# Kernel optimization log

Measured on AMD Instinct MI355X. Metric: run time of the kernel, lower is better.

## Reference

```python
import jax, jax.numpy as jnp
import numpy as np


def setup_inputs() -> dict:
    key = jax.random.key(0)
    k_adj, k_ann, k_b = jax.random.split(key, 3)
    B, N, F = 8, 4096, 64
    # Adjacency: sparse-ish nonnegative matrix (TF version stores it as tf.sparse;
    raw = jax.random.uniform(k_adj, (B, N, N), dtype=jnp.float32)
    adjacent = jnp.where(raw > 0.95, raw, 0.0)
    annotations = jax.random.normal(k_ann, (B, N, F), dtype=jnp.float32)
    bias = jax.random.normal(k_b, (1, 1, F), dtype=jnp.float32)
    return {"adjacent": adjacent, "annotations": annotations, "bias": bias}


def reference(adjacent, annotations, bias):
    # Per-batch sparse @ dense matmul in TF == batched matmul here.
    # adjacent: [B,N,N], annotations: [B,N,F] -> [B,N,F]
    out = jnp.einsum('bnm,bmf->bnf', adjacent, annotations)
    return out + bias
```

## Files before the change

kernel.cpp:

```cpp
#include <hip/hip_runtime.h>
#include <stdint.h>

typedef __bf16 bf16x8 __attribute__((ext_vector_type(8)));
typedef float f32x16 __attribute__((ext_vector_type(16)));

#define NN 4096
#define FF 64
#define BM 64
#define BK 128
#define NSTEP (NN / BK)

__device__ __forceinline__ unsigned short f2bf(float x) {
    unsigned int u = __builtin_bit_cast(unsigned int, x);
    unsigned int r = u + 0x7fffu + ((u >> 16) & 1u);
    return (unsigned short)(r >> 16);
}

__global__ __launch_bounds__(256) void annT_kernel(const float* __restrict__ ann,
                                                   unsigned short* __restrict__ annT) {
    __shared__ unsigned short tile[FF * 66];
    int b = blockIdx.x >> 6;
    int m0 = (blockIdx.x & 63) << 6;
    int t = threadIdx.x;
    int f = t & 63;
    int ml = t >> 6;
    const float* src = ann + ((size_t)(b * NN + m0)) * FF;
#pragma unroll
    for (int it = 0; it < 16; ++it) {
        int m = it * 4 + ml;
        tile[f * 66 + m] = f2bf(src[(size_t)m * FF + f]);
    }
    __syncthreads();
    int m2 = (t & 31) * 2;
    int fr = t >> 5;
    unsigned short* dst = annT + (size_t)b * FF * NN + m0;
#pragma unroll
    for (int it = 0; it < 8; ++it) {
        int fo = it * 8 + fr;
        unsigned int lo = tile[fo * 66 + m2];
        unsigned int hi = tile[fo * 66 + m2 + 1];
        *(unsigned int*)(dst + (size_t)fo * NN + m2) = lo | (hi << 16);
    }
}

__global__ __launch_bounds__(256, 2) void gconv_kernel(const float* __restrict__ A,
                                                       const unsigned short* __restrict__ annT,
                                                       const float* __restrict__ bias,
                                                       float* __restrict__ out) {
    __shared__ unsigned short sA[2][BM * BK];
    __shared__ unsigned short sB[2][FF * BK];

    int bi = blockIdx.x;
    int lw = (bi & 7) * 64 + (bi >> 3);
    int b = lw >> 6;
    int n0 = (lw & 63) << 6;

    int t = threadIdx.x;
    int lane = t & 63;
    int wid = t >> 6;
    int wm = wid >> 1;
    int wf = wid & 1;

    const float* Ab = A + (size_t)b * NN * NN + (size_t)n0 * NN;
    const unsigned short* Tb = annT + (size_t)b * FF * NN;

    float4 ra[8];
    uint4 rb[4];

    auto loadTiles = [&](int s) {
        int k0 = s * BK;
#pragma unroll
        for (int i = 0; i < 8; ++i) {
            int idx = i * 256 + t;
            int row = idx >> 5, c4 = idx & 31;
            ra[i] = *(const float4*)(Ab + (size_t)row * NN + k0 + c4 * 4);
        }
#pragma unroll
        for (int i = 0; i < 4; ++i) {
            int idx = i * 256 + t;
            int fr = idx >> 4, c8 = idx & 15;
            rb[i] = *(const uint4*)(Tb + (size_t)fr * NN + k0 + c8 * 8);
        }
    };

    auto writeLDS = [&](int bufi) {
        unsigned short* pA = sA[bufi];
        unsigned short* pB = sB[bufi];
#pragma unroll
        for (int i = 0; i < 8; ++i) {
            int idx = i * 256 + t;
            int row = idx >> 5, c4 = idx & 31;
            unsigned int byte = (unsigned)(row * 256 + c4 * 8);
            byte ^= (unsigned)((row & 15) << 4);
            ushort4 w;
            w.x = f2bf(ra[i].x);
            w.y = f2bf(ra[i].y);
            w.z = f2bf(ra[i].z);
            w.w = f2bf(ra[i].w);
            *(ushort4*)((char*)pA + byte) = w;
        }
#pragma unroll
        for (int i = 0; i < 4; ++i) {
            int idx = i * 256 + t;
            int fr = idx >> 4, c8 = idx & 15;
            unsigned int byte = (unsigned)(fr * 256 + c8 * 16);
            byte ^= (unsigned)((fr & 15) << 4);
            *(uint4*)((char*)pB + byte) = rb[i];
        }
    };

    int arow = wm * 32 + (lane & 31);
    unsigned aBase = (unsigned)(arow * 256);
    unsigned aswz = (unsigned)((arow & 15) << 4);
    int frow = wf * 32 + (lane & 31);
    unsigned bBase = (unsigned)(frow * 256);
    unsigned bswz = (unsigned)((frow & 15) << 4);
    unsigned kh = (unsigned)((lane >> 5) * 16);

    f32x16 acc = {};

    loadTiles(0);
    writeLDS(0);
    __syncthreads();

    for (int s = 0; s < NSTEP; ++s) {
        int cur = s & 1;
        if (s + 1 < NSTEP) loadTiles(s + 1);
        const char* pA = (const char*)sA[cur];
        const char* pB = (const char*)sB[cur];
#pragma unroll
        for (int ks = 0; ks < 8; ++ks) {
            unsigned ab = (aBase + (unsigned)(ks * 32) + kh) ^ aswz;
            unsigned bb = (bBase + (unsigned)(ks * 32) + kh) ^ bswz;
            bf16x8 af = *(const bf16x8*)(pA + ab);
            bf16x8 bfr = *(const bf16x8*)(pB + bb);
            acc = __builtin_amdgcn_mfma_f32_32x32x16_bf16(af, bfr, acc, 0, 0, 0);
        }
        if (s + 1 < NSTEP) writeLDS((s + 1) & 1);
        __syncthreads();
    }

    float bv = bias[wf * 32 + (lane & 31)];
    float* ob = out + ((size_t)(b * NN + n0 + wm * 32)) * FF + wf * 32 + (lane & 31);
    int rbase = (lane >> 5) * 4;
#pragma unroll
    for (int r = 0; r < 16; ++r) {
        int rowl = (r & 3) + 8 * (r >> 2) + rbase;
        ob[(size_t)rowl * FF] = acc[r] + bv;
    }
}

extern "C" void kernel_launch(void* const* d_in, const int* in_sizes, int n_in,
                              void* d_out, int out_size, void* d_ws, size_t ws_size,
                              hipStream_t stream) {
    const float* adj = (const float*)d_in[0];
    const float* ann = (const float*)d_in[1];
    const float* bias = (const float*)d_in[2];
    float* out = (float*)d_out;
    unsigned short* annT = (unsigned short*)d_ws;

    annT_kernel<<<dim3(8 * (NN / 64)), dim3(256), 0, stream>>>(ann, annT);
    gconv_kernel<<<dim3(8 * (NN / BM)), dim3(256), 0, stream>>>(adj, annT, bias, out);
}
```

Baseline: 686.1 us.

## Replace LDS-tiled GEMM with single-wave register-direct MFMA loads and double buffering

```diff
diff --git a/kernel.cpp b/kernel.cpp
--- a/kernel.cpp
+++ b/kernel.cpp
@@ -6,14 +6,15 @@
 
 #define NN 4096
 #define FF 64
-#define BM 64
-#define BK 128
-#define NSTEP (NN / BK)
 
 __device__ __forceinline__ unsigned short f2bf(float x) {
     unsigned int u = __builtin_bit_cast(unsigned int, x);
     unsigned int r = u + 0x7fffu + ((u >> 16) & 1u);
     return (unsigned short)(r >> 16);
+}
+
+__device__ __forceinline__ unsigned int pk2(float lo, float hi) {
+    return (unsigned int)f2bf(lo) | ((unsigned int)f2bf(hi) << 16);
 }
 
 __global__ __launch_bounds__(256) void annT_kernel(const float* __restrict__ ann,
@@ -43,110 +44,68 @@
     }
 }
 
-__global__ __launch_bounds__(256, 2) void gconv_kernel(const float* __restrict__ A,
-                                                       const unsigned short* __restrict__ annT,
-                                                       const float* __restrict__ bias,
-                                                       float* __restrict__ out) {
-    __shared__ unsigned short sA[2][BM * BK];
-    __shared__ unsigned short sB[2][FF * BK];
+__global__ __launch_bounds__(64) void gconv_kernel(const float* __restrict__ A,
+                                                   const unsigned short* __restrict__ annT,
+                                                   const float* __restrict__ bias,
+                                                   float* __restrict__ out) {
+    int bi = blockIdx.x;
+    int b = bi & 7;
+    int n0 = (bi >> 3) << 5;
+    int lane = threadIdx.x;
+    int r = lane & 31;
+    int h = lane >> 5;
 
-    int bi = blockIdx.x;
-    int lw = (bi & 7) * 64 + (bi >> 3);
-    int b = lw >> 6;
-    int n0 = (lw & 63) << 6;
+    const float* Ap = A + (size_t)b * NN * NN + (size_t)(n0 + r) * NN + h * 8;
+    const unsigned short* B0p = annT + (size_t)b * FF * NN + (size_t)r * NN + h * 8;
+    const unsigned short* B1p = B0p + (size_t)32 * NN;
 
-    int t = threadIdx.x;
-    int lane = t & 63;
-    int wid = t >> 6;
-    int wm = wid >> 1;
-    int wf = wid & 1;
+    f32x16 acc0 = {}, acc1 = {};
 
-    const float* Ab = A + (size_t)b * NN * NN + (size_t)n0 * NN;
-    const unsigned short* Tb = annT + (size_t)b * FF * NN;
+    float4 aA[4][2]; uint4 bA0[4], bA1[4];
+    float4 aB[4][2]; uint4 bB0[4], bB1[4];
 
-    float4 ra[8];
-    uint4 rb[4];
-
-    auto loadTiles = [&](int s) {
-        int k0 = s * BK;
+    auto loadSet = [&](float4 (&a)[4][2], uint4 (&b0)[4], uint4 (&b1)[4], int k0) {
 #pragma unroll
-        for (int i = 0; i < 8; ++i) {
-            int idx = i * 256 + t;
-            int row = idx >> 5, c4 = idx & 31;
-            ra[i] = *(const float4*)(Ab + (size_t)row * NN + k0 + c4 * 4);
+        for (int j = 0; j < 4; ++j) {
+            int k = k0 + j * 16;
+            a[j][0] = *(const float4*)(Ap + k);
+            a[j][1] = *(const float4*)(Ap + k + 4);
+            b0[j] = *(const uint4*)(B0p + k);
+            b1[j] = *(const uint4*)(B1p + k);
         }
+    };
+    auto compSet = [&](float4 (&a)[4][2], uint4 (&b0)[4], uint4 (&b1)[4]) {
 #pragma unroll
-        for (int i = 0; i < 4; ++i) {
-            int idx = i * 256 + t;
-            int fr = idx >> 4, c8 = idx & 15;
-            rb[i] = *(const uint4*)(Tb + (size_t)fr * NN + k0 + c8 * 8);
+        for (int j = 0; j < 4; ++j) {
+            uint4 ap;
+            ap.x = pk2(a[j][0].x, a[j][0].y);
+            ap.y = pk2(a[j][0].z, a[j][0].w);
+            ap.z = pk2(a[j][1].x, a[j][1].y);
+            ap.w = pk2(a[j][1].z, a[j][1].w);
+            bf16x8 af = __builtin_bit_cast(bf16x8, ap);
+            acc0 = __builtin_amdgcn_mfma_f32_32x32x16_bf16(
+                af, __builtin_bit_cast(bf16x8, b0[j]), acc0, 0, 0, 0);
+            acc1 = __builtin_amdgcn_mfma_f32_32x32x16_bf16(
+                af, __builtin_bit_cast(bf16x8, b1[j]), acc1, 0, 0, 0);
         }
     };
 
-    auto writeLDS = [&](int bufi) {
-        unsigned short* pA = sA[bufi];
-        unsigned short* pB = sB[bufi];
-#pragma unroll
-        for (int i = 0; i < 8; ++i) {
-            int idx = i * 256 + t;
-            int row = idx >> 5, c4 = idx & 31;
-            unsigned int byte = (unsigned)(row * 256 + c4 * 8);
-            byte ^= (unsigned)((row & 15) << 4);
-            ushort4 w;
-            w.x = f2bf(ra[i].x);
-            w.y = f2bf(ra[i].y);
-            w.z = f2bf(ra[i].z);
-            w.w = f2bf(ra[i].w);
-            *(ushort4*)((char*)pA + byte) = w;
-        }
-#pragma unroll
-        for (int i = 0; i < 4; ++i) {
-            int idx = i * 256 + t;
-            int fr = idx >> 4, c8 = idx & 15;
-            unsigned int byte = (unsigned)(fr * 256 + c8 * 16);
-            byte ^= (unsigned)((fr & 15) << 4);
-            *(uint4*)((char*)pB + byte) = rb[i];
-        }
-    };
-
-    int arow = wm * 32 + (lane & 31);
-    unsigned aBase = (unsigned)(arow * 256);
-    unsigned aswz = (unsigned)((arow & 15) << 4);
-    int frow = wf * 32 + (lane & 31);
-    unsigned bBase = (unsigned)(frow * 256);
-    unsigned bswz = (unsigned)((frow & 15) << 4);
-    unsigned kh = (unsigned)((lane >> 5) * 16);
-
-    f32x16 acc = {};
-
-    loadTiles(0);
-    writeLDS(0);
-    __syncthreads();
-
-    for (int s = 0; s < NSTEP; ++s) {
-        int cur = s & 1;
-        if (s + 1 < NSTEP) loadTiles(s + 1);
-        const char* pA = (const char*)sA[cur];
-        const char* pB = (const char*)sB[cur];
-#pragma unroll
-        for (int ks = 0; ks < 8; ++ks) {
-            unsigned ab = (aBase + (unsigned)(ks * 32) + kh) ^ aswz;
-            unsigned bb = (bBase + (unsigned)(ks * 32) + kh) ^ bswz;
-            bf16x8 af = *(const bf16x8*)(pA + ab);
-            bf16x8 bfr = *(const bf16x8*)(pB + bb);
-            acc = __builtin_amdgcn_mfma_f32_32x32x16_bf16(af, bfr, acc, 0, 0, 0);
-        }
-        if (s + 1 < NSTEP) writeLDS((s + 1) & 1);
-        __syncthreads();
+    loadSet(aA, bA0, bA1, 0);
+#pragma unroll 1
+    for (int k0 = 0; k0 < NN; k0 += 128) {
+        loadSet(aB, bB0, bB1, k0 + 64);
+        compSet(aA, bA0, bA1);
+        if (k0 + 128 < NN) loadSet(aA, bA0, bA1, k0 + 128);
+        compSet(aB, bB0, bB1);
     }
 
-    float bv = bias[wf * 32 + (lane & 31)];
-    float* ob = out + ((size_t)(b * NN + n0 + wm * 32)) * FF + wf * 32 + (lane & 31);
-    int rbase = (lane >> 5) * 4;
+    float bv0 = bias[r], bv1 = bias[32 + r];
+    float* ob = out + ((size_t)(b * NN + n0)) * FF;
 #pragma unroll
-    for (int r = 0; r < 16; ++r) {
-        int rowl = (r & 3) + 8 * (r >> 2) + rbase;
-        ob[(size_t)rowl * FF] = acc[r] + bv;
+    for (int t = 0; t < 16; ++t) {
+        int rowl = (t & 3) + 8 * (t >> 2) + h * 4;
+        ob[(size_t)rowl * FF + r] = acc0[t] + bv0;
+        ob[(size_t)rowl * FF + 32 + r] = acc1[t] + bv1;
     }
 }
 
@@ -160,5 +119,5 @@
     unsigned short* annT = (unsigned short*)d_ws;
 
     annT_kernel<<<dim3(8 * (NN / 64)), dim3(256), 0, stream>>>(ann, annT);
-    gconv_kernel<<<dim3(8 * (NN / BM)), dim3(256), 0, stream>>>(adj, annT, bias, out);
+    gconv_kernel<<<dim3(8 * (NN / 32)), dim3(64), 0, stream>>>(adj, annT, bias, out);
 }
```

Measured after the change: 729.2 us. 6.3% more time.
